# Kernel optimization log

Hardware: AMD Instinct MI355X
Metric: run time of the kernel (lower is better)

Reference implementation:

```python
import jax, jax.numpy as jnp
import numpy as np

IMG_H = 256; IMG_W = 256; N_PTS = 192
MIN_DEPTH = 3.0; MAX_DEPTH = 9.0
NDC_EXTENT = 1.0; FOCAL = 4.0  # focal length so rays at volume center span ~[-1,1]
EPS = 1e-8; EA_EPS = 1e-10


def setup_inputs() -> dict:
    key = jax.random.key(0)
    image3d = jax.random.uniform(key, (1, 1, 128, 128, 128), dtype=jnp.float32)
    R = jnp.eye(3, dtype=jnp.float32)[None]            # [1,3,3] camera rotation
    T = jnp.array([[0.0, 0.0, 4.0]], dtype=jnp.float32)  # camera center at world (0,0,-4)
    return {"image3d": image3d, "R": R, "T": T}


def _trilinear(vol, pts):
    # vol: [C,D,H,W]; pts: [N,3] xyz in [-1,1]; align_corners=True, zero padding
    C, D, H, W = vol.shape
    fx = (pts[:, 0] + 1.0) * 0.5 * (W - 1)
    fy = (pts[:, 1] + 1.0) * 0.5 * (H - 1)
    fz = (pts[:, 2] + 1.0) * 0.5 * (D - 1)
    x0 = jnp.floor(fx); y0 = jnp.floor(fy); z0 = jnp.floor(fz)
    wx = fx - x0; wy = fy - y0; wz = fz - z0
    out = jnp.zeros((pts.shape[0], C), vol.dtype)
    for dz in (0, 1):
        for dy in (0, 1):
            for dx in (0, 1):
                xi = x0 + dx; yi = y0 + dy; zi = z0 + dz
                w = ((wx if dx else 1.0 - wx) * (wy if dy else 1.0 - wy)
                     * (wz if dz else 1.0 - wz))
                valid = ((xi >= 0) & (xi <= W - 1) & (yi >= 0) & (yi <= H - 1)
                         & (zi >= 0) & (zi <= D - 1))
                xc = jnp.clip(xi, 0, W - 1).astype(jnp.int32)
                yc = jnp.clip(yi, 0, H - 1).astype(jnp.int32)
                zc = jnp.clip(zi, 0, D - 1).astype(jnp.int32)
                vals = vol[:, zc, yc, xc]          # [C,N] gather
                out = out + (w * valid).astype(vol.dtype)[:, None] * vals.T
    return out                                      # [N,C]


def reference(image3d, R, T):
    B = image3d.shape[0]
    features = jnp.repeat(image3d, 3, axis=1)                 # [B,3,D,H,W]
    densities = jnp.ones_like(image3d) / N_PTS                # [B,1,D,H,W]
    vol4 = jnp.concatenate([features, densities], axis=1)     # [B,4,D,H,W]
    # NDC pixel grid + depths along each ray
    ys = jnp.linspace(1.0, -1.0, IMG_H)
    xs = jnp.linspace(1.0, -1.0, IMG_W)
    yg, xg = jnp.meshgrid(ys, xs, indexing="ij")              # [H,W]
    depths = jnp.linspace(MIN_DEPTH, MAX_DEPTH, N_PTS)        # [P]
    x_cam = xg[..., None] * depths / FOCAL                    # [H,W,P]
    y_cam = yg[..., None] * depths / FOCAL
    z_cam = jnp.broadcast_to(depths, x_cam.shape)
    pts_cam = jnp.stack([x_cam, y_cam, z_cam], axis=-1)       # [H,W,P,3]
    # X_cam = X_world @ R + T  =>  X_world = (X_cam - T) @ R^T
    pts_world = jnp.einsum("bhwpj,bij->bhwpi",
                           pts_cam[None] - T[:, None, None, None, :], R)
    local = pts_world / NDC_EXTENT                            # volume local coords in [-1,1]
    sampled = jax.vmap(_trilinear)(vol4, local.reshape(B, -1, 3))  # [B,N,4]
    sampled = sampled.reshape(B, IMG_H, IMG_W, N_PTS, 4)
    feats = sampled[..., :3]
    dens = sampled[..., 3]                                    # [B,H,W,P]
    # EmissionAbsorption raymarcher (shifted cumprod of transmittance)
    t = (1.0 + EA_EPS) - dens
    cp = jnp.cumprod(t, axis=-1)
    absorption = jnp.concatenate([jnp.ones_like(cp[..., :1]), cp[..., :-1]], axis=-1)
    weights = dens * absorption
    rgb = jnp.einsum("bhwp,bhwpc->bhwc", weights, feats)      # [B,H,W,3]
    opac = 1.0 - jnp.prod(1.0 - dens, axis=-1, keepdims=True)
    rgba = jnp.concatenate([rgb, opac], axis=-1)              # [B,H,W,4]
    screen = jnp.transpose(rgba, (0, 3, 1, 2))                # [B,4,H,W]
    gray = screen.mean(axis=1, keepdims=True)                 # [B,1,H,W]
    # normalized(standardized(x))  (torch std is unbiased -> ddof=1)
    std = (gray - gray.mean()) / (jnp.std(gray, ddof=1) + EPS)
    out = (std - std.min() + EPS) / (std.max() - std.min() + EPS)
    return out
```

## Files before the change

### kernel.cpp

```cpp
#include <hip/hip_runtime.h>
#include <math.h>

#define N_PIX (256 * 256)
#define N_PTS 192
#define SEGS 4
#define PIX_PER_BLK 64
#define N_BLK (N_PIX / PIX_PER_BLK)

__global__ __launch_bounds__(256) void render_kernel(
    const float* __restrict__ vol,
    const float* __restrict__ Rm,
    const float* __restrict__ Tv,
    float* __restrict__ out,
    float* __restrict__ part)
{
    const int tid = threadIdx.x;
    const int seg = tid & (SEGS - 1);
    const int pix = blockIdx.x * PIX_PER_BLK + (tid >> 2);
    const int h = pix >> 8;
    const int w = pix & 255;
    const float yg = 1.0f - (2.0f / 255.0f) * (float)h;
    const float xg = 1.0f - (2.0f / 255.0f) * (float)w;

    const float r00 = Rm[0], r01 = Rm[1], r02 = Rm[2];
    const float r10 = Rm[3], r11 = Rm[4], r12 = Rm[5];
    const float r20 = Rm[6], r21 = Rm[7], r22 = Rm[8];
    const float t0 = Tv[0], t1 = Tv[1], t2 = Tv[2];

    const float a0 = 0.25f * (r00 * xg + r01 * yg) + r02;
    const float a1 = 0.25f * (r10 * xg + r11 * yg) + r12;
    const float a2 = 0.25f * (r20 * xg + r21 * yg) + r22;
    const float b0 = -(r00 * t0 + r01 * t1 + r02 * t2);
    const float b1 = -(r10 * t0 + r11 * t1 + r12 * t2);
    const float b2 = -(r20 * t0 + r21 * t1 + r22 * t2);

    const float LIM = 1.0f + 2.0f / 127.0f + 1e-4f;
    float dlo = 3.0f, dhi = 9.0f;
    {
        const float aa[3] = {a0, a1, a2};
        const float bb[3] = {b0, b1, b2};
        #pragma unroll
        for (int k = 0; k < 3; ++k) {
            const float a = aa[k], b = bb[k];
            if (fabsf(a) > 1e-12f) {
                const float i0 = (-LIM - b) / a;
                const float i1 = ( LIM - b) / a;
                dlo = fmaxf(dlo, fminf(i0, i1));
                dhi = fminf(dhi, fmaxf(i0, i1));
            } else if (fabsf(b) >= LIM) {
                dhi = -1e30f;
            }
        }
    }
    const float step = 6.0f / 191.0f;
    const float rstep = 191.0f / 6.0f;
    int plo = (int)ceilf((dlo - 3.0f) * rstep - 1e-3f);
    int phi = (int)floorf((dhi - 3.0f) * rstep + 1e-3f);
    plo = max(plo, 0);
    phi = min(phi, N_PTS - 1);
    int len = phi - plo + 1;
    if (len < 0) len = 0;
    const int chunk = (len + SEGS - 1) >> 2;
    const int iBeg = plo + seg * chunk;
    const int iEnd = min(iBeg + chunk, plo + len);

    float P = 1.0f;
    float U = 1.0f;
    float S = 0.0f;

    #pragma unroll 2
    for (int p = iBeg; p < iEnd; ++p) {
        const float d = fmaf(step, (float)p, 3.0f);
        const float fx = (fmaf(a0, d, b0) + 1.0f) * 63.5f;
        const float fy = (fmaf(a1, d, b1) + 1.0f) * 63.5f;
        const float fz = (fmaf(a2, d, b2) + 1.0f) * 63.5f;
        const float x0f = floorf(fx), y0f = floorf(fy), z0f = floorf(fz);
        const float wx = fx - x0f, wy = fy - y0f, wz = fz - z0f;
        const int ix = (int)x0f, iy = (int)y0f, iz = (int)z0f;
        const float ax0 = (ix >= 0  && ix <= 127) ? (1.0f - wx) : 0.0f;
        const float ax1 = (ix >= -1 && ix <= 126) ? wx : 0.0f;
        const float ay0 = (iy >= 0  && iy <= 127) ? (1.0f - wy) : 0.0f;
        const float ay1 = (iy >= -1 && iy <= 126) ? wy : 0.0f;
        const float az0 = (iz >= 0  && iz <= 127) ? (1.0f - wz) : 0.0f;
        const float az1 = (iz >= -1 && iz <= 126) ? wz : 0.0f;
        const float s = (ax0 + ax1) * (ay0 + ay1) * (az0 + az1);
        const float dens = s * (1.0f / 192.0f);
        const int xc0 = min(max(ix, 0), 127);
        const int xc1 = min(max(ix + 1, 0), 127);
        const int yc0 = min(max(iy, 0), 127);
        const int yc1 = min(max(iy + 1, 0), 127);
        const int zc0 = min(max(iz, 0), 127);
        const int zc1 = min(max(iz + 1, 0), 127);
        const float* q00 = vol + (zc0 * 128 + yc0) * 128;
        const float* q01 = vol + (zc0 * 128 + yc1) * 128;
        const float* q10 = vol + (zc1 * 128 + yc0) * 128;
        const float* q11 = vol + (zc1 * 128 + yc1) * 128;
        const float v000 = q00[xc0], v001 = q00[xc1];
        const float v010 = q01[xc0], v011 = q01[xc1];
        const float v100 = q10[xc0], v101 = q10[xc1];
        const float v110 = q11[xc0], v111 = q11[xc1];
        const float feat =
            az0 * (ay0 * (ax0 * v000 + ax1 * v001) + ay1 * (ax0 * v010 + ax1 * v011)) +
            az1 * (ay0 * (ax0 * v100 + ax1 * v101) + ay1 * (ax0 * v110 + ax1 * v111));
        S = fmaf(dens * P, feat, S);
        P *= (1.0f + 1e-10f - dens);
        U *= (1.0f - dens);
    }

    float inc = P;
    #pragma unroll
    for (int off = 1; off < SEGS; off <<= 1) {
        const float v = __shfl_up(inc, off, SEGS);
        if (seg >= off) inc *= v;
    }
    float excl = __shfl_up(inc, 1, SEGS);
    if (seg == 0) excl = 1.0f;
    float wS = excl * S;
    #pragma unroll
    for (int off = 1; off < SEGS; off <<= 1) {
        wS += __shfl_xor(wS, off, SEGS);
        U  *= __shfl_xor(U, off, SEGS);
    }

    const bool leader = (seg == 0);
    float g = 0.0f;
    if (leader) {
        g = (3.0f * wS + (1.0f - U)) * 0.25f;
        out[pix] = g;
    }

    float vs = leader ? g : 0.0f;
    float vq = leader ? g * g : 0.0f;
    float vmn = leader ? g : 1e30f;
    float vmx = leader ? g : -1e30f;
    #pragma unroll
    for (int off = 4; off < 64; off <<= 1) {
        vs += __shfl_xor(vs, off);
        vq += __shfl_xor(vq, off);
        vmn = fminf(vmn, __shfl_xor(vmn, off));
        vmx = fmaxf(vmx, __shfl_xor(vmx, off));
    }
    __shared__ float s_s[4], s_q[4], s_n[4], s_x[4];
    const int wave = tid >> 6;
    const int lane = tid & 63;
    if (lane == 0) { s_s[wave] = vs; s_q[wave] = vq; s_n[wave] = vmn; s_x[wave] = vmx; }
    __syncthreads();
    if (tid == 0) {
        part[blockIdx.x]             = s_s[0] + s_s[1] + s_s[2] + s_s[3];
        part[N_BLK + blockIdx.x]     = s_q[0] + s_q[1] + s_q[2] + s_q[3];
        part[2 * N_BLK + blockIdx.x] = fminf(fminf(s_n[0], s_n[1]), fminf(s_n[2], s_n[3]));
        part[3 * N_BLK + blockIdx.x] = fmaxf(fmaxf(s_x[0], s_x[1]), fmaxf(s_x[2], s_x[3]));
    }
}

__global__ __launch_bounds__(256) void finish_kernel(
    float* __restrict__ out,
    const float* __restrict__ part)
{
    const int tid = threadIdx.x;
    __shared__ float s_s[4], s_q[4], s_n[4], s_x[4];
    __shared__ float s_fin[4];

    float fs  = part[tid]               + part[tid + 256]
              + part[tid + 512]         + part[tid + 768];
    float fq  = part[N_BLK + tid]       + part[N_BLK + tid + 256]
              + part[N_BLK + tid + 512] + part[N_BLK + tid + 768];
    float fn  = fminf(fminf(part[2 * N_BLK + tid],       part[2 * N_BLK + tid + 256]),
                      fminf(part[2 * N_BLK + tid + 512], part[2 * N_BLK + tid + 768]));
    float fx2 = fmaxf(fmaxf(part[3 * N_BLK + tid],       part[3 * N_BLK + tid + 256]),
                      fmaxf(part[3 * N_BLK + tid + 512], part[3 * N_BLK + tid + 768]));
    #pragma unroll
    for (int off = 1; off < 64; off <<= 1) {
        fs += __shfl_xor(fs, off);
        fq += __shfl_xor(fq, off);
        fn  = fminf(fn,  __shfl_xor(fn, off));
        fx2 = fmaxf(fx2, __shfl_xor(fx2, off));
    }
    const int wave = tid >> 6;
    const int lane = tid & 63;
    if (lane == 0) { s_s[wave] = fs; s_q[wave] = fq; s_n[wave] = fn; s_x[wave] = fx2; }
    __syncthreads();
    if (tid == 0) {
        const float tsum = s_s[0] + s_s[1] + s_s[2] + s_s[3];
        const float tsq  = s_q[0] + s_q[1] + s_q[2] + s_q[3];
        const float tmn  = fminf(fminf(s_n[0], s_n[1]), fminf(s_n[2], s_n[3]));
        const float tmx  = fmaxf(fmaxf(s_x[0], s_x[1]), fmaxf(s_x[2], s_x[3]));
        const float N = (float)N_PIX;
        const float mean = tsum / N;
        float var = (tsq - N * mean * mean) / (N - 1.0f);
        if (var < 0.0f) var = 0.0f;
        const float denom = sqrtf(var) + 1e-8f;
        s_fin[0] = mean;
        s_fin[1] = denom;
        s_fin[2] = (tmn - mean) / denom;
        s_fin[3] = (tmx - mean) / denom;
    }
    __syncthreads();

    const float mean = s_fin[0];
    const float rdenom = 1.0f / s_fin[1];
    const float smin = s_fin[2];
    const float rrange = 1.0f / (s_fin[3] - smin + 1e-8f);
    const int i = blockIdx.x * 256 + tid;
    const float sv = (out[i] - mean) * rdenom;
    out[i] = (sv - smin + 1e-8f) * rrange;
}

extern "C" void kernel_launch(void* const* d_in, const int* in_sizes, int n_in,
                              void* d_out, int out_size, void* d_ws, size_t ws_size,
                              hipStream_t stream)
{
    const float* vol = (const float*)d_in[0];
    const float* Rm  = (const float*)d_in[1];
    const float* Tv  = (const float*)d_in[2];
    float* out = (float*)d_out;
    float* part = (float*)d_ws;

    hipLaunchKernelGGL(render_kernel, dim3(N_BLK), dim3(256), 0, stream,
                       vol, Rm, Tv, out, part);
    hipLaunchKernelGGL(finish_kernel, dim3(N_PIX / 256), dim3(256), 0, stream,
                       out, part);
}
```

Baseline: 87.24 us.

## Split each ray across 8 waves on 8x8 pixel tiles, combine via LDS

Each block now covers an 8x8 pixel tile, and each of 8 wavefronts marches one eighth of the ray segment for all 64 pixels. Neighbouring lanes therefore sample spatially adjacent points, which should improve cache locality for the trilinear gathers. Per-segment partial transmittance and accumulation go through shared memory, and one wave does the sequential combine and block reduction. Doubling the segments per ray adds parallelism but also more per-thread setup and a larger block, and only one wave does the final combine.

```diff
diff --git a/kernel.cpp b/kernel.cpp
--- a/kernel.cpp
+++ b/kernel.cpp
@@ -3,11 +3,12 @@
 
 #define N_PIX (256 * 256)
 #define N_PTS 192
-#define SEGS 4
-#define PIX_PER_BLK 64
-#define N_BLK (N_PIX / PIX_PER_BLK)
-
-__global__ __launch_bounds__(256) void render_kernel(
+#define SEGS 8
+#define TILE_PIX 64
+#define N_BLK (N_PIX / TILE_PIX)
+#define THREADS (TILE_PIX * SEGS)
+
+__global__ __launch_bounds__(THREADS) void render_kernel(
     const float* __restrict__ vol,
     const float* __restrict__ Rm,
     const float* __restrict__ Tv,
@@ -15,10 +16,12 @@
     float* __restrict__ part)
 {
     const int tid = threadIdx.x;
-    const int seg = tid & (SEGS - 1);
-    const int pix = blockIdx.x * PIX_PER_BLK + (tid >> 2);
-    const int h = pix >> 8;
-    const int w = pix & 255;
+    const int seg = tid >> 6;
+    const int l   = tid & 63;
+    const int tr  = blockIdx.x >> 5;
+    const int tc  = blockIdx.x & 31;
+    const int h = tr * 8 + (l >> 3);
+    const int w = tc * 8 + (l & 7);
     const float yg = 1.0f - (2.0f / 255.0f) * (float)h;
     const float xg = 1.0f - (2.0f / 255.0f) * (float)w;
 
@@ -60,7 +63,7 @@
     phi = min(phi, N_PTS - 1);
     int len = phi - plo + 1;
     if (len < 0) len = 0;
-    const int chunk = (len + SEGS - 1) >> 2;
+    const int chunk = (len + SEGS - 1) >> 3;
     const int iBeg = plo + seg * chunk;
     const int iEnd = min(iBeg + chunk, plo + len);
 
@@ -107,49 +110,39 @@
         U *= (1.0f - dens);
     }
 
-    float inc = P;
-    #pragma unroll
-    for (int off = 1; off < SEGS; off <<= 1) {
-        const float v = __shfl_up(inc, off, SEGS);
-        if (seg >= off) inc *= v;
-    }
-    float excl = __shfl_up(inc, 1, SEGS);
-    if (seg == 0) excl = 1.0f;
-    float wS = excl * S;
-    #pragma unroll
-    for (int off = 1; off < SEGS; off <<= 1) {
-        wS += __shfl_xor(wS, off, SEGS);
-        U  *= __shfl_xor(U, off, SEGS);
-    }
-
-    const bool leader = (seg == 0);
-    float g = 0.0f;
-    if (leader) {
-        g = (3.0f * wS + (1.0f - U)) * 0.25f;
-        out[pix] = g;
-    }
-
-    float vs = leader ? g : 0.0f;
-    float vq = leader ? g * g : 0.0f;
-    float vmn = leader ? g : 1e30f;
-    float vmx = leader ? g : -1e30f;
-    #pragma unroll
-    for (int off = 4; off < 64; off <<= 1) {
-        vs += __shfl_xor(vs, off);
-        vq += __shfl_xor(vq, off);
-        vmn = fminf(vmn, __shfl_xor(vmn, off));
-        vmx = fmaxf(vmx, __shfl_xor(vmx, off));
-    }
-    __shared__ float s_s[4], s_q[4], s_n[4], s_x[4];
-    const int wave = tid >> 6;
-    const int lane = tid & 63;
-    if (lane == 0) { s_s[wave] = vs; s_q[wave] = vq; s_n[wave] = vmn; s_x[wave] = vmx; }
+    __shared__ float sP[SEGS][TILE_PIX];
+    __shared__ float sU[SEGS][TILE_PIX];
+    __shared__ float sS[SEGS][TILE_PIX];
+    sP[seg][l] = P;
+    sU[seg][l] = U;
+    sS[seg][l] = S;
     __syncthreads();
-    if (tid == 0) {
-        part[blockIdx.x]             = s_s[0] + s_s[1] + s_s[2] + s_s[3];
-        part[N_BLK + blockIdx.x]     = s_q[0] + s_q[1] + s_q[2] + s_q[3];
-        part[2 * N_BLK + blockIdx.x] = fminf(fminf(s_n[0], s_n[1]), fminf(s_n[2], s_n[3]));
-        part[3 * N_BLK + blockIdx.x] = fmaxf(fmaxf(s_x[0], s_x[1]), fmaxf(s_x[2], s_x[3]));
+
+    if (tid < TILE_PIX) {
+        float absorb = 1.0f, uAll = 1.0f, wS = 0.0f;
+        #pragma unroll
+        for (int s = 0; s < SEGS; ++s) {
+            wS = fmaf(absorb, sS[s][l], wS);
+            absorb *= sP[s][l];
+            uAll   *= sU[s][l];
+        }
+        const float g = (3.0f * wS + (1.0f - uAll)) * 0.25f;
+        out[h * 256 + w] = g;
+
+        float vs = g, vq = g * g, vmn = g, vmx = g;
+        #pragma unroll
+        for (int off = 1; off < 64; off <<= 1) {
+            vs += __shfl_xor(vs, off);
+            vq += __shfl_xor(vq, off);
+            vmn = fminf(vmn, __shfl_xor(vmn, off));
+            vmx = fmaxf(vmx, __shfl_xor(vmx, off));
+        }
+        if (l == 0) {
+            part[blockIdx.x]             = vs;
+            part[N_BLK + blockIdx.x]     = vq;
+            part[2 * N_BLK + blockIdx.x] = vmn;
+            part[3 * N_BLK + blockIdx.x] = vmx;
+        }
     }
 }
 
@@ -216,7 +209,7 @@
     float* out = (float*)d_out;
     float* part = (float*)d_ws;
 
-    hipLaunchKernelGGL(render_kernel, dim3(N_BLK), dim3(256), 0, stream,
+    hipLaunchKernelGGL(render_kernel, dim3(N_BLK), dim3(THREADS), 0, stream,
                        vol, Rm, Tv, out, part);
     hipLaunchKernelGGL(finish_kernel, dim3(N_PIX / 256), dim3(256), 0, stream,
                        out, part);
```

Measured after the change: 88.42 us. No clear change (+1.4%).
